# Optimization experiments

Hardware: AMD Instinct MI355X
Metric: run time of the kernel (lower is better)

The kernel has to match this reference:

```python
import jax, jax.numpy as jnp
import numpy as np

D_MODEL = 1536
NUM_EXPERTS = 64
TOP_K = 2
D_HIDDEN = 512
LN_EPS = 1e-5


def setup_inputs() -> dict:
    key = jax.random.key(0)
    ks = jax.random.split(key, 6)
    B, S = 2, 2048
    x = jax.random.normal(ks[0], (B, S, D_MODEL), dtype=jnp.float32)
    # router: nn.Linear(d_model, num_experts, bias=False) -> weight [E, D]
    Wr = jax.random.normal(ks[1], (NUM_EXPERTS, D_MODEL), dtype=jnp.float32) / np.sqrt(D_MODEL)
    # per-expert MLP weights, torch Linear layout: w1 [H, D], w2 [D, H], stacked over experts
    W1 = jax.random.normal(ks[2], (NUM_EXPERTS, D_HIDDEN, D_MODEL), dtype=jnp.float32) / np.sqrt(D_MODEL)
    W2 = jax.random.normal(ks[3], (NUM_EXPERTS, D_MODEL, D_HIDDEN), dtype=jnp.float32) / np.sqrt(D_HIDDEN)
    gamma = jnp.ones((D_MODEL,), dtype=jnp.float32)
    beta = jnp.zeros((D_MODEL,), dtype=jnp.float32)
    return {"x": x, "Wr": Wr, "W1": W1, "W2": W2, "gamma": gamma, "beta": beta}


def reference(x, Wr, W1, W2, gamma, beta):
    B, S, D = x.shape
    xf = x.reshape(-1, D)                                   # [T, D]
    logits = xf @ Wr.T                                      # [T, E]
    top_w, top_idx = jax.lax.top_k(logits, TOP_K)           # [T, K]
    top_w = jax.nn.softmax(top_w, axis=-1)                  # softmax over selected k
    # combine[t, e] = sum_k top_w[t, k] * 1{top_idx[t,k]==e}; zero for unselected experts,
    # so dense all-expert compute below is mathematically identical to the masked loop.
    onehot = jax.nn.one_hot(top_idx, NUM_EXPERTS, dtype=xf.dtype)   # [T, K, E]
    combine = jnp.einsum("tk,tke->te", top_w, onehot)       # [T, E]
    h = jax.nn.silu(jnp.einsum("td,ehd->teh", xf, W1))      # [T, E, H]
    hw = h * combine[:, :, None]                            # weight before second GEMM
    out = jnp.einsum("teh,edh->td", hw, W2)                 # [T, D]
    # LayerNorm (eps=1e-5, affine)
    mu = jnp.mean(out, axis=-1, keepdims=True)
    var = jnp.mean(jnp.square(out - mu), axis=-1, keepdims=True)
    out = (out - mu) * jax.lax.rsqrt(var + LN_EPS) * gamma + beta
    return out.reshape(B, S, D)
```

## Files before the change

### kernel.cpp

```cpp
#include <hip/hip_runtime.h>
#include <hip/hip_bf16.h>

#define D_MODEL 1536
#define NEXP    64
#define D_HID   512
#define NTOK    4096
#define NT1     (D_MODEL / 64)
#define NT2     (D_HID / 64)
#define MT      192

typedef __attribute__((ext_vector_type(8))) short short8;
typedef __attribute__((ext_vector_type(4))) float f32x4;

__device__ __forceinline__ unsigned short f2bf(float f) {
  unsigned u = __builtin_bit_cast(unsigned, f);
  u += 0x7FFFu + ((u >> 16) & 1u);
  return (unsigned short)(u >> 16);
}
__device__ __forceinline__ unsigned pk2(float a, float b) {
  return (unsigned)f2bf(a) | ((unsigned)f2bf(b) << 16);
}
__device__ __forceinline__ float bf2f(unsigned short u) {
  return __builtin_bit_cast(float, ((unsigned)u) << 16);
}

__device__ __forceinline__ void gl16(const void* g, void* s) {
  __builtin_amdgcn_global_load_lds(
      (const __attribute__((address_space(1))) unsigned int*)g,
      (__attribute__((address_space(3))) unsigned int*)s, 16, 0, 0);
}

#define WAITV(N)  asm volatile("s_waitcnt vmcnt(" #N ")" ::: "memory")
#define WAITL0    asm volatile("s_waitcnt lgkmcnt(0)" ::: "memory")
#define SBAR      __builtin_amdgcn_s_barrier()
#define SCHED0    __builtin_amdgcn_sched_barrier(0)


__global__ void zero_small_kernel(int* __restrict__ counts) {
  counts[threadIdx.x] = 0;
}


__global__ __launch_bounds__(256) void router_kernel(const float* __restrict__ x,
    const float* __restrict__ Wr, int* __restrict__ topidx, float* __restrict__ topw,
    int* __restrict__ counts, unsigned short* __restrict__ xb)
{
  __shared__ float xs[8][32];
  __shared__ float wst[32][64];
  const int tid  = threadIdx.x;
  const int lane = tid & 63;
  const int wv   = tid >> 6;
  const int t0   = blockIdx.x * 8;

  float acc[2][4];
  #pragma unroll
  for (int i = 0; i < 2; ++i)
    #pragma unroll
    for (int j = 0; j < 4; ++j) acc[i][j] = 0.f;

  for (int k0 = 0; k0 < D_MODEL; k0 += 32) {
    __syncthreads();
    {
      int r = tid >> 5, c = tid & 31;
      float xv = x[(long)(t0 + r) * D_MODEL + k0 + c];
      xs[r][c] = xv;
      xb[(long)(t0 + r) * D_MODEL + k0 + c] = f2bf(xv);
    }
    {
      int e = tid >> 2, q = tid & 3;
      const float* wp = Wr + (long)e * D_MODEL + k0 + q * 8;
      float4 v0 = *(const float4*)wp;
      float4 v1 = *(const float4*)(wp + 4);
      int kk = q * 8;
      wst[kk + 0][e] = v0.x; wst[kk + 1][e] = v0.y; wst[kk + 2][e] = v0.z; wst[kk + 3][e] = v0.w;
      wst[kk + 4][e] = v1.x; wst[kk + 5][e] = v1.y; wst[kk + 6][e] = v1.z; wst[kk + 7][e] = v1.w;
    }
    __syncthreads();
    #pragma unroll
    for (int k = 0; k < 32; k += 4) {
      #pragma unroll
      for (int kb = 0; kb < 4; ++kb) {
        float wvv = wst[k + kb][lane];
        #pragma unroll
        for (int i = 0; i < 2; ++i)
          acc[i][kb] = fmaf(xs[wv * 2 + i][k + kb], wvv, acc[i][kb]);
      }
    }
  }
  float lg[2];
  #pragma unroll
  for (int i = 0; i < 2; ++i) lg[i] = (acc[i][0] + acc[i][1]) + (acc[i][2] + acc[i][3]);

  for (int i = 0; i < 2; ++i) {
    float v = lg[i];
    float v0 = v; int e0 = lane;
    #pragma unroll
    for (int off = 32; off > 0; off >>= 1) {
      float ov = __shfl_xor(v0, off);
      int   oe = __shfl_xor(e0, off);
      if (ov > v0 || (ov == v0 && oe < e0)) { v0 = ov; e0 = oe; }
    }
    float v1 = (lane == e0) ? -3.0e38f : v;
    int e1 = lane;
    #pragma unroll
    for (int off = 32; off > 0; off >>= 1) {
      float ov = __shfl_xor(v1, off);
      int   oe = __shfl_xor(e1, off);
      if (ov > v1 || (ov == v1 && oe < e1)) { v1 = ov; e1 = oe; }
    }
    if (lane == 0) {
      int t = t0 + wv * 2 + i;
      float w0 = 1.f / (1.f + expf(v1 - v0));
      topidx[t * 2]     = e0;
      topidx[t * 2 + 1] = e1;
      topw[t * 2]       = w0;
      topw[t * 2 + 1]   = 1.f - w0;
      atomicAdd(&counts[e0], 1);
      atomicAdd(&counts[e1], 1);
    }
  }
}


__global__ void scan_kernel(const int* __restrict__ counts, int* __restrict__ offs,
                            int* __restrict__ cursor)
{
  int e = threadIdx.x;
  int c = counts[e];
  int xx = c;
  #pragma unroll
  for (int off = 1; off < 64; off <<= 1) {
    int y = __shfl_up(xx, off);
    if (e >= off) xx += y;
  }
  offs[e + 1] = xx;
  if (e == 0) offs[0] = 0;
  cursor[e] = 0;
}

__global__ void scatter_kernel(const int* __restrict__ topidx, const float* __restrict__ topw,
    const int* __restrict__ offs, int* __restrict__ cursor,
    int* __restrict__ perm, float* __restrict__ wgt, int* __restrict__ tok2slot)
{
  int t = blockIdx.x * blockDim.x + threadIdx.x;
  if (t >= NTOK) return;
  #pragma unroll
  for (int k = 0; k < 2; ++k) {
    int e = topidx[t * 2 + k];
    float w = topw[t * 2 + k];
    int pos = atomicAdd(&cursor[e], 1);
    int slot = offs[e] + pos;
    perm[slot] = t;
    wgt[slot] = w;
    tok2slot[t * 2 + k] = slot;
  }
}


__global__ __launch_bounds__(256, 2) void ffn1_kernel(
    const unsigned short* __restrict__ xb, const float* __restrict__ W1,
    const int* __restrict__ offs, const int* __restrict__ perm,
    const float* __restrict__ wgt, unsigned short* __restrict__ hbuf)
{
  const int e  = blockIdx.x;
  const int nc = blockIdx.y;
  const int cnt = offs[e + 1] - offs[e];
  if (cnt == 0) return;

  __shared__ unsigned short Abuf[2][MT * 64];
  __shared__ unsigned short Bbuf[2][64 * 64];

  const int tid  = threadIdx.x;
  const int lane = tid & 63;
  const int wv   = tid >> 6;

  const int qB = tid & 15;
  const int rB = tid >> 4;
  const float* bptr[4];
  #pragma unroll
  for (int p = 0; p < 4; ++p)
    bptr[p] = W1 + ((long)e * D_HID + nc * 64 + p * 16 + rB) * D_MODEL + qB * 4;

  int arow[3], brow[4];
  int physA[2][3], physB[2][4];
  #pragma unroll
  for (int mi = 0; mi < 3; ++mi) {
    arow[mi] = wv * 48 + mi * 16 + (lane & 15);
    #pragma unroll
    for (int ks = 0; ks < 2; ++ks)
      physA[ks][mi] = (ks * 4 + (lane >> 4)) ^ (arow[mi] & 7);
  }
  #pragma unroll
  for (int ni = 0; ni < 4; ++ni) {
    brow[ni] = ni * 16 + (lane & 15);
    #pragma unroll
    for (int ks = 0; ks < 2; ++ks)
      physB[ks][ni] = (ks * 4 + (lane >> 4)) ^ (brow[ni] & 7);
  }
  const int lslot = (lane & 7) ^ (lane >> 3);

  for (int m0 = 0; m0 < cnt; m0 += MT) {
    const int base = offs[e] + m0;
    const int mcnt = min(MT, cnt - m0);

    const unsigned short* gptrA[6];
    #pragma unroll
    for (int j = 0; j < 6; ++j) {
      int pr = (wv * 6 + j) * 8 + (lane >> 3);
      if (pr >= mcnt) pr = mcnt - 1;
      gptrA[j] = xb + (long)perm[base + pr] * D_MODEL + lslot * 8;
    }

    f32x4 acc[3][4];
    #pragma unroll
    for (int i = 0; i < 3; ++i)
      #pragma unroll
      for (int j = 0; j < 4; ++j) acc[i][j] = (f32x4)0.f;

    float4 bregA[4], bregB[4];

    auto ISSUE = [&](int t, float4* br, unsigned short* Ab) {
      const int k0 = t * 64;
      SCHED0;
      #pragma unroll
      for (int p = 0; p < 4; ++p) br[p] = *(const float4*)(bptr[p] + k0);
      SCHED0;
      #pragma unroll
      for (int j = 0; j < 6; ++j)
        gl16(gptrA[j] + k0, Ab + (wv * 6 + j) * 512);
      SCHED0;
    };
    auto WRITE_B = [&](const float4* br, unsigned short* B_) {
      #pragma unroll
      for (int p = 0; p < 4; ++p) {
        int rr = p * 16 + rB;
        unsigned lo = pk2(br[p].x, br[p].y);
        unsigned hi = pk2(br[p].z, br[p].w);
        int ph = (qB >> 1) ^ (rr & 7);
        *(uint2*)(B_ + rr * 64 + ph * 8 + (qB & 1) * 4) = make_uint2(lo, hi);
      }
    };
    auto COMPUTE = [&](const unsigned short* A_, const unsigned short* B_) {
      #pragma unroll
      for (int ks = 0; ks < 2; ++ks) {
        short8 a[3], bb[4];
        #pragma unroll
        for (int mi = 0; mi < 3; ++mi)
          a[mi] = *(const short8*)(A_ + arow[mi] * 64 + physA[ks][mi] * 8);
        #pragma unroll
        for (int ni = 0; ni < 4; ++ni)
          bb[ni] = *(const short8*)(B_ + brow[ni] * 64 + physB[ks][ni] * 8);
        #pragma unroll
        for (int mi = 0; mi < 3; ++mi)
          #pragma unroll
          for (int ni = 0; ni < 4; ++ni)
            acc[mi][ni] = __builtin_amdgcn_mfma_f32_16x16x32_bf16(a[mi], bb[ni], acc[mi][ni], 0, 0, 0);
      }
    };

    ISSUE(0, bregA, Abuf[0]);
    WAITV(6);
    WRITE_B(bregA, Bbuf[0]);
    ISSUE(1, bregB, Abuf[1]);
    WAITV(10);
    WAITL0;
    SBAR;

    #pragma unroll 1
    for (int t = 0; t < NT1; t += 2) {
      COMPUTE(Abuf[0], Bbuf[0]);
      SBAR;
      WAITV(6);
      WRITE_B(bregB, Bbuf[1]);
      if (t + 2 < NT1) { ISSUE(t + 2, bregA, Abuf[0]); WAITV(10); }
      else             { WAITV(0); }
      WAITL0;
      SBAR;
      COMPUTE(Abuf[1], Bbuf[1]);
      SBAR;
      if (t + 2 < NT1) {
        WAITV(6);
        WRITE_B(bregA, Bbuf[0]);
        if (t + 3 < NT1) { ISSUE(t + 3, bregB, Abuf[1]); WAITV(10); }
        else             { WAITV(0); }
        WAITL0;
        SBAR;
      }
    }

    const int rsub = (lane >> 4) * 4;
    const int csub = lane & 15;
    #pragma unroll
    for (int mi = 0; mi < 3; ++mi) {
      #pragma unroll
      for (int rg = 0; rg < 4; ++rg) {
        int r = wv * 48 + mi * 16 + rsub + rg;
        if (r < mcnt) {
          float wt = wgt[base + r];
          unsigned short* hrow = hbuf + (long)(base + r) * D_HID + nc * 64 + csub;
          #pragma unroll
          for (int ni = 0; ni < 4; ++ni) {
            float v = acc[mi][ni][rg];
            float sv = v / (1.f + __expf(-v)) * wt;
            hrow[ni * 16] = f2bf(sv);
          }
        }
      }
    }
    __syncthreads();
  }
}


__global__ __launch_bounds__(256, 2) void ffn2_kernel(
    const unsigned short* __restrict__ hbuf, const float* __restrict__ W2,
    const int* __restrict__ offs, unsigned short* __restrict__ sbuf)
{
  const int e  = blockIdx.x;
  const int nc = blockIdx.y;
  const int cnt = offs[e + 1] - offs[e];
  if (cnt == 0) return;

  __shared__ unsigned short Abuf[2][MT * 64];
  __shared__ unsigned short Bbuf[2][64 * 64];

  const int tid  = threadIdx.x;
  const int lane = tid & 63;
  const int wv   = tid >> 6;

  const int qB = tid & 15;
  const int rB = tid >> 4;
  const float* bptr[4];
  #pragma unroll
  for (int p = 0; p < 4; ++p)
    bptr[p] = W2 + ((long)e * D_MODEL + nc * 64 + p * 16 + rB) * D_HID + qB * 4;

  int arow[3], brow[4];
  int physA[2][3], physB[2][4];
  #pragma unroll
  for (int mi = 0; mi < 3; ++mi) {
    arow[mi] = wv * 48 + mi * 16 + (lane & 15);
    #pragma unroll
    for (int ks = 0; ks < 2; ++ks)
      physA[ks][mi] = (ks * 4 + (lane >> 4)) ^ (arow[mi] & 7);
  }
  #pragma unroll
  for (int ni = 0; ni < 4; ++ni) {
    brow[ni] = ni * 16 + (lane & 15);
    #pragma unroll
    for (int ks = 0; ks < 2; ++ks)
      physB[ks][ni] = (ks * 4 + (lane >> 4)) ^ (brow[ni] & 7);
  }
  const int lslot = (lane & 7) ^ (lane >> 3);

  for (int m0 = 0; m0 < cnt; m0 += MT) {
    const int base = offs[e] + m0;
    const int mcnt = min(MT, cnt - m0);

    const unsigned short* gptrA[6];
    #pragma unroll
    for (int j = 0; j < 6; ++j) {
      int pr = (wv * 6 + j) * 8 + (lane >> 3);
      if (pr >= mcnt) pr = mcnt - 1;
      gptrA[j] = hbuf + (long)(base + pr) * D_HID + lslot * 8;
    }

    f32x4 acc[3][4];
    #pragma unroll
    for (int i = 0; i < 3; ++i)
      #pragma unroll
      for (int j = 0; j < 4; ++j) acc[i][j] = (f32x4)0.f;

    float4 bregA[4], bregB[4];

    auto ISSUE = [&](int t, float4* br, unsigned short* Ab) {
      const int k0 = t * 64;
      SCHED0;
      #pragma unroll
      for (int p = 0; p < 4; ++p) br[p] = *(const float4*)(bptr[p] + k0);
      SCHED0;
      #pragma unroll
      for (int j = 0; j < 6; ++j)
        gl16(gptrA[j] + k0, Ab + (wv * 6 + j) * 512);
      SCHED0;
    };
    auto WRITE_B = [&](const float4* br, unsigned short* B_) {
      #pragma unroll
      for (int p = 0; p < 4; ++p) {
        int rr = p * 16 + rB;
        unsigned lo = pk2(br[p].x, br[p].y);
        unsigned hi = pk2(br[p].z, br[p].w);
        int ph = (qB >> 1) ^ (rr & 7);
        *(uint2*)(B_ + rr * 64 + ph * 8 + (qB & 1) * 4) = make_uint2(lo, hi);
      }
    };
    auto COMPUTE = [&](const unsigned short* A_, const unsigned short* B_) {
      #pragma unroll
      for (int ks = 0; ks < 2; ++ks) {
        short8 a[3], bb[4];
        #pragma unroll
        for (int mi = 0; mi < 3; ++mi)
          a[mi] = *(const short8*)(A_ + arow[mi] * 64 + physA[ks][mi] * 8);
        #pragma unroll
        for (int ni = 0; ni < 4; ++ni)
          bb[ni] = *(const short8*)(B_ + brow[ni] * 64 + physB[ks][ni] * 8);
        #pragma unroll
        for (int mi = 0; mi < 3; ++mi)
          #pragma unroll
          for (int ni = 0; ni < 4; ++ni)
            acc[mi][ni] = __builtin_amdgcn_mfma_f32_16x16x32_bf16(a[mi], bb[ni], acc[mi][ni], 0, 0, 0);
      }
    };

    ISSUE(0, bregA, Abuf[0]);
    WAITV(6);
    WRITE_B(bregA, Bbuf[0]);
    ISSUE(1, bregB, Abuf[1]);
    WAITV(10);
    WAITL0;
    SBAR;

    #pragma unroll 1
    for (int t = 0; t < NT2; t += 2) {
      COMPUTE(Abuf[0], Bbuf[0]);
      SBAR;
      WAITV(6);
      WRITE_B(bregB, Bbuf[1]);
      if (t + 2 < NT2) { ISSUE(t + 2, bregA, Abuf[0]); WAITV(10); }
      else             { WAITV(0); }
      WAITL0;
      SBAR;
      COMPUTE(Abuf[1], Bbuf[1]);
      SBAR;
      if (t + 2 < NT2) {
        WAITV(6);
        WRITE_B(bregA, Bbuf[0]);
        if (t + 3 < NT2) { ISSUE(t + 3, bregB, Abuf[1]); WAITV(10); }
        else             { WAITV(0); }
        WAITL0;
        SBAR;
      }
    }

    unsigned short* fds = &Abuf[0][0];
    const int rsub = (lane >> 4) * 4;
    const int csub = lane & 15;
    #pragma unroll
    for (int mi = 0; mi < 3; ++mi) {
      #pragma unroll
      for (int rg = 0; rg < 4; ++rg) {
        int r = wv * 48 + mi * 16 + rsub + rg;
        #pragma unroll
        for (int ni = 0; ni < 4; ++ni)
          fds[r * 64 + ni * 16 + csub] = f2bf(acc[mi][ni][rg]);
      }
    }
    __syncthreads();
    #pragma unroll
    for (int q = 0; q < 6; ++q) {
      int idx = q * 256 + tid;
      int row = idx >> 3, c8 = idx & 7;
      if (row < mcnt)
        *(uint4*)(sbuf + (long)(base + row) * D_MODEL + nc * 64 + c8 * 8) =
            *(const uint4*)(fds + row * 64 + c8 * 8);
    }
    __syncthreads();
  }
}


__global__ __launch_bounds__(192) void ln_kernel(const unsigned short* __restrict__ sbuf,
    const int* __restrict__ tok2slot, float* __restrict__ out,
    const float* __restrict__ gamma, const float* __restrict__ beta)
{
  const int tid = threadIdx.x;
  const int t = blockIdx.x;
  const long r0 = (long)tok2slot[t * 2]     * D_MODEL;
  const long r1 = (long)tok2slot[t * 2 + 1] * D_MODEL;

  uint4 u0 = *(const uint4*)(sbuf + r0 + tid * 8);
  uint4 u1 = *(const uint4*)(sbuf + r1 + tid * 8);
  float v[8];
  {
    const unsigned* p0 = &u0.x;
    const unsigned* p1 = &u1.x;
    #pragma unroll
    for (int i = 0; i < 4; ++i) {
      v[i * 2]     = bf2f((unsigned short)(p0[i] & 0xFFFFu)) + bf2f((unsigned short)(p1[i] & 0xFFFFu));
      v[i * 2 + 1] = bf2f((unsigned short)(p0[i] >> 16))     + bf2f((unsigned short)(p1[i] >> 16));
    }
  }

  float s = 0.f, sq = 0.f;
  #pragma unroll
  for (int i = 0; i < 8; ++i) { s += v[i]; sq += v[i] * v[i]; }
  #pragma unroll
  for (int off = 32; off > 0; off >>= 1) {
    s  += __shfl_xor(s, off);
    sq += __shfl_xor(sq, off);
  }
  __shared__ float ss[3], sqs[3];
  int wv = tid >> 6;
  if ((tid & 63) == 0) { ss[wv] = s; sqs[wv] = sq; }
  __syncthreads();
  s  = ss[0] + ss[1] + ss[2];
  sq = sqs[0] + sqs[1] + sqs[2];
  const float inv = 1.f / (float)D_MODEL;
  float mu  = s * inv;
  float var = sq * inv - mu * mu;
  float rs  = 1.f / sqrtf(var + 1e-5f);

  float4 g1 = *(const float4*)(gamma + tid * 8);
  float4 g2 = *(const float4*)(gamma + tid * 8 + 4);
  float4 b1v = *(const float4*)(beta + tid * 8);
  float4 b2v = *(const float4*)(beta + tid * 8 + 4);
  float4 a, b;
  a.x = (v[0] - mu) * rs * g1.x + b1v.x;
  a.y = (v[1] - mu) * rs * g1.y + b1v.y;
  a.z = (v[2] - mu) * rs * g1.z + b1v.z;
  a.w = (v[3] - mu) * rs * g1.w + b1v.w;
  b.x = (v[4] - mu) * rs * g2.x + b2v.x;
  b.y = (v[5] - mu) * rs * g2.y + b2v.y;
  b.z = (v[6] - mu) * rs * g2.z + b2v.z;
  b.w = (v[7] - mu) * rs * g2.w + b2v.w;
  float* row = out + (long)t * D_MODEL;
  *(float4*)(row + tid * 8)     = a;
  *(float4*)(row + tid * 8 + 4) = b;
}


extern "C" void kernel_launch(void* const* d_in, const int* in_sizes, int n_in,
                              void* d_out, int out_size, void* d_ws, size_t ws_size,
                              hipStream_t stream) {
  const float* x     = (const float*)d_in[0];
  const float* Wr    = (const float*)d_in[1];
  const float* W1    = (const float*)d_in[2];
  const float* W2    = (const float*)d_in[3];
  const float* gamma = (const float*)d_in[4];
  const float* beta  = (const float*)d_in[5];
  float* out = (float*)d_out;

  char* ws = (char*)d_ws;
  unsigned short* xb     = (unsigned short*)(ws + 0);
  unsigned short* hbuf   = (unsigned short*)(ws + 12582912);
  unsigned short* sbuf   = (unsigned short*)(ws + 20971520);
  int*   topidx   = (int*)  (ws + 46137344);
  float* topw     = (float*)(ws + 46170112);
  int*   counts   = (int*)  (ws + 46202880);
  int*   cursor   = (int*)  (ws + 46203136);
  int*   offs     = (int*)  (ws + 46203392);
  int*   tok2slot = (int*)  (ws + 46203904);
  int*   perm     = (int*)  (ws + 46236672);
  float* wgt      = (float*)(ws + 46269440);

  hipLaunchKernelGGL(zero_small_kernel, dim3(1), dim3(64), 0, stream, counts);
  hipLaunchKernelGGL(router_kernel, dim3(NTOK / 8), dim3(256), 0, stream, x, Wr, topidx, topw, counts, xb);
  hipLaunchKernelGGL(scan_kernel, dim3(1), dim3(64), 0, stream, counts, offs, cursor);
  hipLaunchKernelGGL(scatter_kernel, dim3(NTOK / 256), dim3(256), 0, stream, topidx, topw, offs, cursor, perm, wgt, tok2slot);
  hipLaunchKernelGGL(ffn1_kernel, dim3(NEXP, 8), dim3(256), 0, stream, xb, W1, offs, perm, wgt, hbuf);
  hipLaunchKernelGGL(ffn2_kernel, dim3(NEXP, 24), dim3(256), 0, stream, hbuf, W2, offs, sbuf);
  hipLaunchKernelGGL(ln_kernel, dim3(NTOK), dim3(192), 0, stream, sbuf, tok2slot, out, gamma, beta);
}
```

Baseline: 243.4 us.

## Rework router loads, swap grid order, add MFMA priority, stage FFN1 stores

The router now loads each token's full x row into shared memory once with float4 reads, and each lane reads its expert's Wr row straight from global memory, which removes the per-32-element sync loop. The FFN grids are transposed so the column-chunk blocks of one expert are launched next to each other. s_setprio is raised around the MFMA bursts. The FFN1 epilogue stages its bf16 results in LDS and writes them out as 16-byte coalesced stores instead of scattered 2-byte stores. The cost is an extra barrier and LDS round trip in the epilogue, and uncoalesced per-lane Wr row reads in the router.

```diff
diff --git a/kernel.cpp b/kernel.cpp
--- a/kernel.cpp
+++ b/kernel.cpp
@@ -45,47 +45,49 @@
     const float* __restrict__ Wr, int* __restrict__ topidx, float* __restrict__ topw,
     int* __restrict__ counts, unsigned short* __restrict__ xb)
 {
-  __shared__ float xs[8][32];
-  __shared__ float wst[32][64];
+  __shared__ float xs[8][D_MODEL];
   const int tid  = threadIdx.x;
   const int lane = tid & 63;
   const int wv   = tid >> 6;
   const int t0   = blockIdx.x * 8;
 
+  #pragma unroll
+  for (int rr = 0; rr < 2; ++rr) {
+    int r = wv * 2 + rr;
+    const float* xrow = x + (long)(t0 + r) * D_MODEL;
+    unsigned short* xbrow = xb + (long)(t0 + r) * D_MODEL;
+    #pragma unroll
+    for (int j = 0; j < 6; ++j) {
+      int c = j * 256 + lane * 4;
+      float4 v = *(const float4*)(xrow + c);
+      *(float4*)(&xs[r][c]) = v;
+      *(uint2*)(xbrow + c) = make_uint2(pk2(v.x, v.y), pk2(v.z, v.w));
+    }
+  }
+  __syncthreads();
+
+  const float* wrow = Wr + (long)lane * D_MODEL;
   float acc[2][4];
   #pragma unroll
   for (int i = 0; i < 2; ++i)
     #pragma unroll
     for (int j = 0; j < 4; ++j) acc[i][j] = 0.f;
 
-  for (int k0 = 0; k0 < D_MODEL; k0 += 32) {
-    __syncthreads();
-    {
-      int r = tid >> 5, c = tid & 31;
-      float xv = x[(long)(t0 + r) * D_MODEL + k0 + c];
-      xs[r][c] = xv;
-      xb[(long)(t0 + r) * D_MODEL + k0 + c] = f2bf(xv);
-    }
-    {
-      int e = tid >> 2, q = tid & 3;
-      const float* wp = Wr + (long)e * D_MODEL + k0 + q * 8;
-      float4 v0 = *(const float4*)wp;
-      float4 v1 = *(const float4*)(wp + 4);
-      int kk = q * 8;
-      wst[kk + 0][e] = v0.x; wst[kk + 1][e] = v0.y; wst[kk + 2][e] = v0.z; wst[kk + 3][e] = v0.w;
-      wst[kk + 4][e] = v1.x; wst[kk + 5][e] = v1.y; wst[kk + 6][e] = v1.z; wst[kk + 7][e] = v1.w;
-    }
-    __syncthreads();
-    #pragma unroll
-    for (int k = 0; k < 32; k += 4) {
-      #pragma unroll
-      for (int kb = 0; kb < 4; ++kb) {
-        float wvv = wst[k + kb][lane];
-        #pragma unroll
-        for (int i = 0; i < 2; ++i)
-          acc[i][kb] = fmaf(xs[wv * 2 + i][k + kb], wvv, acc[i][kb]);
-      }
-    }
+  const float* x0p = &xs[wv * 2][0];
+  const float* x1p = &xs[wv * 2 + 1][0];
+  #pragma unroll 4
+  for (int k = 0; k < D_MODEL; k += 4) {
+    float4 w4 = *(const float4*)(wrow + k);
+    float4 x0 = *(const float4*)(x0p + k);
+    float4 x1 = *(const float4*)(x1p + k);
+    acc[0][0] = fmaf(x0.x, w4.x, acc[0][0]);
+    acc[0][1] = fmaf(x0.y, w4.y, acc[0][1]);
+    acc[0][2] = fmaf(x0.z, w4.z, acc[0][2]);
+    acc[0][3] = fmaf(x0.w, w4.w, acc[0][3]);
+    acc[1][0] = fmaf(x1.x, w4.x, acc[1][0]);
+    acc[1][1] = fmaf(x1.y, w4.y, acc[1][1]);
+    acc[1][2] = fmaf(x1.z, w4.z, acc[1][2]);
+    acc[1][3] = fmaf(x1.w, w4.w, acc[1][3]);
   }
   float lg[2];
   #pragma unroll
@@ -162,8 +164,8 @@
     const int* __restrict__ offs, const int* __restrict__ perm,
     const float* __restrict__ wgt, unsigned short* __restrict__ hbuf)
 {
-  const int e  = blockIdx.x;
-  const int nc = blockIdx.y;
+  const int nc = blockIdx.x;
+  const int e  = blockIdx.y;
   const int cnt = offs[e + 1] - offs[e];
   if (cnt == 0) return;
 
@@ -250,11 +252,13 @@
         #pragma unroll
         for (int ni = 0; ni < 4; ++ni)
           bb[ni] = *(const short8*)(B_ + brow[ni] * 64 + physB[ks][ni] * 8);
+        __builtin_amdgcn_s_setprio(1);
         #pragma unroll
         for (int mi = 0; mi < 3; ++mi)
           #pragma unroll
           for (int ni = 0; ni < 4; ++ni)
             acc[mi][ni] = __builtin_amdgcn_mfma_f32_16x16x32_bf16(a[mi], bb[ni], acc[mi][ni], 0, 0, 0);
+        __builtin_amdgcn_s_setprio(0);
       }
     };
 
@@ -288,6 +292,7 @@
       }
     }
 
+    unsigned short* fds = &Abuf[0][0];
     const int rsub = (lane >> 4) * 4;
     const int csub = lane & 15;
     #pragma unroll
@@ -295,17 +300,23 @@
       #pragma unroll
       for (int rg = 0; rg < 4; ++rg) {
         int r = wv * 48 + mi * 16 + rsub + rg;
-        if (r < mcnt) {
-          float wt = wgt[base + r];
-          unsigned short* hrow = hbuf + (long)(base + r) * D_HID + nc * 64 + csub;
-          #pragma unroll
-          for (int ni = 0; ni < 4; ++ni) {
-            float v = acc[mi][ni][rg];
-            float sv = v / (1.f + __expf(-v)) * wt;
-            hrow[ni * 16] = f2bf(sv);
-          }
+        float wt = (r < mcnt) ? wgt[base + r] : 0.f;
+        #pragma unroll
+        for (int ni = 0; ni < 4; ++ni) {
+          float v = acc[mi][ni][rg];
+          float sv = v / (1.f + __expf(-v)) * wt;
+          fds[r * 64 + ni * 16 + csub] = f2bf(sv);
         }
       }
+    }
+    __syncthreads();
+    #pragma unroll
+    for (int q = 0; q < 6; ++q) {
+      int idx = q * 256 + tid;
+      int row = idx >> 3, c8 = idx & 7;
+      if (row < mcnt)
+        *(uint4*)(hbuf + (long)(base + row) * D_HID + nc * 64 + c8 * 8) =
+            *(const uint4*)(fds + row * 64 + c8 * 8);
     }
     __syncthreads();
   }
@@ -316,8 +327,8 @@
     const unsigned short* __restrict__ hbuf, const float* __restrict__ W2,
     const int* __restrict__ offs, unsigned short* __restrict__ sbuf)
 {
-  const int e  = blockIdx.x;
-  const int nc = blockIdx.y;
+  const int nc = blockIdx.x;
+  const int e  = blockIdx.y;
   const int cnt = offs[e + 1] - offs[e];
   if (cnt == 0) return;
 
@@ -404,11 +415,13 @@
         #pragma unroll
         for (int ni = 0; ni < 4; ++ni)
           bb[ni] = *(const short8*)(B_ + brow[ni] * 64 + physB[ks][ni] * 8);
+        __builtin_amdgcn_s_setprio(1);
         #pragma unroll
         for (int mi = 0; mi < 3; ++mi)
           #pragma unroll
           for (int ni = 0; ni < 4; ++ni)
             acc[mi][ni] = __builtin_amdgcn_mfma_f32_16x16x32_bf16(a[mi], bb[ni], acc[mi][ni], 0, 0, 0);
+        __builtin_amdgcn_s_setprio(0);
       }
     };
 
@@ -557,7 +570,7 @@
   hipLaunchKernelGGL(router_kernel, dim3(NTOK / 8), dim3(256), 0, stream, x, Wr, topidx, topw, counts, xb);
   hipLaunchKernelGGL(scan_kernel, dim3(1), dim3(64), 0, stream, counts, offs, cursor);
   hipLaunchKernelGGL(scatter_kernel, dim3(NTOK / 256), dim3(256), 0, stream, topidx, topw, offs, cursor, perm, wgt, tok2slot);
-  hipLaunchKernelGGL(ffn1_kernel, dim3(NEXP, 8), dim3(256), 0, stream, xb, W1, offs, perm, wgt, hbuf);
-  hipLaunchKernelGGL(ffn2_kernel, dim3(NEXP, 24), dim3(256), 0, stream, hbuf, W2, offs, sbuf);
+  hipLaunchKernelGGL(ffn1_kernel, dim3(8, NEXP), dim3(256), 0, stream, xb, W1, offs, perm, wgt, hbuf);
+  hipLaunchKernelGGL(ffn2_kernel, dim3(24, NEXP), dim3(256), 0, stream, hbuf, W2, offs, sbuf);
   hipLaunchKernelGGL(ln_kernel, dim3(NTOK), dim3(192), 0, stream, sbuf, tok2slot, out, gamma, beta);
 }
```

Result: slower. 279.5 us (+14.8%).
